# Optimization experiments

Hardware: AMD Instinct MI355X
Metric: run time of the kernel (lower is better)

The kernel has to match this reference:

```python
import jax, jax.numpy as jnp
import numpy as np

# Production-scale dims (ScanNet-like 3D instance segmentation, Mask3D-style matcher)
B = 4            # scenes per batch (equal-size segments; offset = cumulative N)
N = 65536        # points per scene
Q = 400          # instance queries
NUM_CLASSES = 20 # semantic classes
M = 64           # max GT instances per scene
COST_CLASS = 1.0
COST_MASK = 1.0
COST_DICE = 1.0


def setup_inputs() -> dict:
    key = jax.random.key(0)
    k1, k2, k3, k4 = jax.random.split(key, 4)
    outputs_mask = jax.random.normal(k1, (B, N, Q), dtype=jnp.float32)
    outputs_class = jax.random.normal(k2, (B, Q, NUM_CLASSES), dtype=jnp.float32)
    instance = jax.random.randint(k3, (B, N), 0, M, dtype=jnp.int32)
    segment = jax.random.randint(k4, (B, N), 0, NUM_CLASSES, dtype=jnp.int32)
    return {
        'outputs_mask': outputs_mask,
        'outputs_class': outputs_class,
        'instance': instance,
        'segment': segment,
    }


def _cost_matrix(out_mask_nq, out_cls, inst, seg):
    # out_mask_nq: [N, Q] mask logits; out_cls: [Q, C]; inst, seg: [N] int
    out_mask = out_mask_nq.T                      # [Q, N]
    out_seg = jax.nn.softmax(out_cls, axis=-1)    # [Q, C]

    # F.one_hot(inst + 1).T[1:] with labels in [0, M) == one_hot(inst, M).T
    tgt = jax.nn.one_hot(inst, M, dtype=jnp.float32).T  # [M, N]

    # semantic label per instance: (tgt_mask * tgt_segm).max(1)
    inst_seg = jnp.max(tgt * seg.astype(jnp.float32)[None, :], axis=1).astype(jnp.int32)  # [M]
    cost_class = 1.0 - out_seg[:, inst_seg]       # [Q, M]

    # batch_sigmoid_ce_loss: BCEwithLogits(x,1)=softplus(-x), BCEwithLogits(x,0)=softplus(x)
    inv_hw = 1.0 / N
    pos = jax.nn.softplus(-out_mask) * inv_hw     # [Q, N]
    neg = jax.nn.softplus(out_mask) * inv_hw      # [Q, N]
    cost_mask = (jnp.einsum('qn,mn->qm', pos, tgt)
                 + jnp.einsum('qn,mn->qm', neg, 1.0 - tgt))  # [Q, M]

    # batch_dice_loss
    sig = jax.nn.sigmoid(out_mask)                # [Q, N]
    numerator = 2.0 * jnp.einsum('qn,mn->qm', sig, tgt)
    denominator = sig.sum(-1)[:, None] + tgt.sum(-1)[None, :]
    cost_dice = 1.0 - (numerator + 1.0) / (denominator + 1.0)

    return COST_MASK * cost_mask + COST_CLASS * cost_class + COST_DICE * cost_dice


def reference(outputs_mask, outputs_class, instance, segment):
    # vmap over scenes (equal-size segments replace the per-batch offset loop)
    return jax.vmap(_cost_matrix)(outputs_mask, outputs_class, instance, segment)  # [B, Q, M]
```

## Files before the change

kernel.cpp:

```cpp
#include <hip/hip_runtime.h>
#include <hip/hip_bf16.h>

#define B_ 4
#define N_ 65536
#define Q_ 400
#define C_ 20
#define M_ 64
#define QT 64
#define CHUNK 1024
#define NCHUNK (N_ / CHUNK)
#define NQT ((Q_ + QT - 1) / QT)

#define SX 8192.0f
#define SS 32768.0f
#define SN 8192.0f

__global__ __launch_bounds__(256) void stats_kernel(const int* __restrict__ inst,
                                                    const int* __restrict__ seg,
                                                    int* __restrict__ cnt_g,
                                                    int* __restrict__ smax_g) {
    int b = blockIdx.x >> 4;
    int chunk = blockIdx.x & 15;
    __shared__ int scnt[M_];
    __shared__ int smax[M_];
    int tid = threadIdx.x;
    if (tid < M_) { scnt[tid] = 0; smax[tid] = 0; }
    __syncthreads();
    int base = b * N_ + chunk * 4096;
    for (int i = 0; i < 4096; i += 256) {
        int m = inst[base + tid + i];
        int s = seg[base + tid + i];
        atomicAdd(&scnt[m], 1);
        atomicMax(&smax[m], s);
    }
    __syncthreads();
    if (tid < M_) {
        atomicAdd(&cnt_g[b * M_ + tid], scnt[tid]);
        atomicMax(&smax_g[b * M_ + tid], smax[tid]);
    }
}

__global__ __launch_bounds__(512) void bin_kernel(const float* __restrict__ mask,
                                                  const int* __restrict__ inst,
                                                  int* __restrict__ xsum,
                                                  int* __restrict__ ssum,
                                                  int* __restrict__ negsum) {
    int chunk = blockIdx.x, qt = blockIdx.y, b = blockIdx.z;
    int qbase = qt * QT;
    __shared__ int xs[M_][QT + 1];
    __shared__ int ss[M_][QT + 1];
    __shared__ int linst[CHUNK];
    int tid = threadIdx.x;
    for (int i = tid; i < M_ * (QT + 1); i += 512) {
        (&xs[0][0])[i] = 0;
        (&ss[0][0])[i] = 0;
    }
    const int2* ip = (const int2*)(inst + b * N_ + chunk * CHUNK);
    ((int2*)linst)[tid] = ip[tid];
    __syncthreads();

    int lane = tid & 63, wave = tid >> 6;
    int r = lane >> 4, c = lane & 15;
    int q0 = qbase + 4 * c;
    bool qok = (q0 < Q_);
    int lq = 4 * c;

    float n0 = 0.f, n1 = 0.f, n2 = 0.f, n3 = 0.f;
    int lnbase = wave * 4 + r;
    const float* mbase = mask + ((size_t)b * N_ + (size_t)chunk * CHUNK) * Q_ + q0;

    if (qok) {
        for (int i = 0; i < CHUNK / 32; i += 2) {
            int ln0 = lnbase + i * 32;
            int ln1 = ln0 + 32;
            float4 xa = *(const float4*)(mbase + (size_t)ln0 * Q_);
            float4 xb = *(const float4*)(mbase + (size_t)ln1 * Q_);
            int m0 = linst[ln0];
            int m1 = linst[ln1];

            float ea0 = __expf(xa.x), ea1 = __expf(xa.y), ea2 = __expf(xa.z), ea3 = __expf(xa.w);
            float eb0 = __expf(xb.x), eb1 = __expf(xb.y), eb2 = __expf(xb.z), eb3 = __expf(xb.w);
            float ta0 = 1.f + ea0, ta1 = 1.f + ea1, ta2 = 1.f + ea2, ta3 = 1.f + ea3;
            float tb0 = 1.f + eb0, tb1 = 1.f + eb1, tb2 = 1.f + eb2, tb3 = 1.f + eb3;
            float sa0 = ea0 * __builtin_amdgcn_rcpf(ta0);
            float sa1 = ea1 * __builtin_amdgcn_rcpf(ta1);
            float sa2 = ea2 * __builtin_amdgcn_rcpf(ta2);
            float sa3 = ea3 * __builtin_amdgcn_rcpf(ta3);
            float sb0 = eb0 * __builtin_amdgcn_rcpf(tb0);
            float sb1 = eb1 * __builtin_amdgcn_rcpf(tb1);
            float sb2 = eb2 * __builtin_amdgcn_rcpf(tb2);
            float sb3 = eb3 * __builtin_amdgcn_rcpf(tb3);

            atomicAdd(&xs[m0][lq + 0], __float2int_rn(xa.x * SX));
            atomicAdd(&xs[m0][lq + 1], __float2int_rn(xa.y * SX));
            atomicAdd(&xs[m0][lq + 2], __float2int_rn(xa.z * SX));
            atomicAdd(&xs[m0][lq + 3], __float2int_rn(xa.w * SX));
            atomicAdd(&ss[m0][lq + 0], (int)__float2uint_rn(sa0 * SS));
            atomicAdd(&ss[m0][lq + 1], (int)__float2uint_rn(sa1 * SS));
            atomicAdd(&ss[m0][lq + 2], (int)__float2uint_rn(sa2 * SS));
            atomicAdd(&ss[m0][lq + 3], (int)__float2uint_rn(sa3 * SS));
            atomicAdd(&xs[m1][lq + 0], __float2int_rn(xb.x * SX));
            atomicAdd(&xs[m1][lq + 1], __float2int_rn(xb.y * SX));
            atomicAdd(&xs[m1][lq + 2], __float2int_rn(xb.z * SX));
            atomicAdd(&xs[m1][lq + 3], __float2int_rn(xb.w * SX));
            atomicAdd(&ss[m1][lq + 0], (int)__float2uint_rn(sb0 * SS));
            atomicAdd(&ss[m1][lq + 1], (int)__float2uint_rn(sb1 * SS));
            atomicAdd(&ss[m1][lq + 2], (int)__float2uint_rn(sb2 * SS));
            atomicAdd(&ss[m1][lq + 3], (int)__float2uint_rn(sb3 * SS));

            n0 += __logf(ta0) + __logf(tb0);
            n1 += __logf(ta1) + __logf(tb1);
            n2 += __logf(ta2) + __logf(tb2);
            n3 += __logf(ta3) + __logf(tb3);
        }
    }

    n0 += __shfl_xor(n0, 16); n0 += __shfl_xor(n0, 32);
    n1 += __shfl_xor(n1, 16); n1 += __shfl_xor(n1, 32);
    n2 += __shfl_xor(n2, 16); n2 += __shfl_xor(n2, 32);
    n3 += __shfl_xor(n3, 16); n3 += __shfl_xor(n3, 32);
    if (r == 0 && qok) {
        atomicAdd(&negsum[b * Q_ + q0 + 0], __float2int_rn(n0 * SN));
        atomicAdd(&negsum[b * Q_ + q0 + 1], __float2int_rn(n1 * SN));
        atomicAdd(&negsum[b * Q_ + q0 + 2], __float2int_rn(n2 * SN));
        atomicAdd(&negsum[b * Q_ + q0 + 3], __float2int_rn(n3 * SN));
    }
    __syncthreads();

    for (int idx = tid; idx < M_ * QT; idx += 512) {
        int m = idx & (M_ - 1);
        int lqq = idx >> 6;
        int q = qbase + lqq;
        if (q < Q_) {
            atomicAdd(&xsum[((b * Q_ + q) << 6) + m], xs[m][lqq]);
            atomicAdd(&ssum[((b * Q_ + q) << 6) + m], ss[m][lqq]);
        }
    }
}

__global__ __launch_bounds__(64) void final_kernel(const float* __restrict__ cls_in,
                                                   const int* __restrict__ xsum,
                                                   const int* __restrict__ ssum,
                                                   const int* __restrict__ negsum,
                                                   const int* __restrict__ cnt_g,
                                                   const int* __restrict__ smax_g,
                                                   float* __restrict__ out) {
    int bq = blockIdx.x;
    int b = bq / Q_;
    int m = threadIdx.x;
    float Xs = (float)xsum[(bq << 6) + m] * (1.0f / SX);
    float Ss = (float)ssum[(bq << 6) + m] * (1.0f / SS);
    float sigsum = Ss;
    for (int off = 32; off; off >>= 1) sigsum += __shfl_xor(sigsum, off);

    __shared__ float cls[C_];
    if (m < C_) cls[m] = cls_in[bq * C_ + m];
    __syncthreads();
    float mx = cls[0];
    for (int i = 1; i < C_; ++i) mx = fmaxf(mx, cls[i]);
    float se = 0.f;
    for (int i = 0; i < C_; ++i) se += __expf(cls[i] - mx);
    int label = smax_g[b * M_ + m];
    float p = __expf(cls[label] - mx) / se;

    float negf = (float)negsum[bq] * (1.0f / SN);
    float cm = (negf - Xs) * (1.f / (float)N_);
    float cd = 1.f - (2.f * Ss + 1.f) / (sigsum + (float)cnt_g[b * M_ + m] + 1.f);
    out[(bq << 6) + m] = cm + (1.f - p) + cd;
}

extern "C" void kernel_launch(void* const* d_in, const int* in_sizes, int n_in,
                              void* d_out, int out_size, void* d_ws, size_t ws_size,
                              hipStream_t stream) {
    const float* mask = (const float*)d_in[0];
    const float* cls  = (const float*)d_in[1];
    const int*   inst = (const int*)d_in[2];
    const int*   seg  = (const int*)d_in[3];
    float* out = (float*)d_out;

    int* xsum   = (int*)d_ws;
    int* ssum   = xsum + B_ * Q_ * M_;
    int* negsum = ssum + B_ * Q_ * M_;
    int* cnt_g  = negsum + B_ * Q_;
    int* smax_g = cnt_g + B_ * M_;

    size_t zbytes = (size_t)(2 * B_ * Q_ * M_ + B_ * Q_ + 2 * B_ * M_) * 4;
    hipMemsetAsync(d_ws, 0, zbytes, stream);

    stats_kernel<<<B_ * 16, 256, 0, stream>>>(inst, seg, cnt_g, smax_g);
    bin_kernel<<<dim3(NCHUNK, NQT, B_), 512, 0, stream>>>(mask, inst, xsum, ssum, negsum);
    final_kernel<<<B_ * Q_, 64, 0, stream>>>(cls, xsum, ssum, negsum, cnt_g, smax_g, out);
}
```

Before: 644.2 us.

## Counting-sort points by instance per chunk to replace LDS atomics with register reductions

```diff
diff --git a/kernel.cpp b/kernel.cpp
--- a/kernel.cpp
+++ b/kernel.cpp
@@ -7,133 +7,169 @@
 #define C_ 20
 #define M_ 64
 #define QT 64
-#define CHUNK 1024
+#define CHUNK 2048
 #define NCHUNK (N_ / CHUNK)
 #define NQT ((Q_ + QT - 1) / QT)
+#define OFFSTRIDE (M_ + 2)
 
 #define SX 8192.0f
 #define SS 32768.0f
 #define SN 8192.0f
 
-__global__ __launch_bounds__(256) void stats_kernel(const int* __restrict__ inst,
-                                                    const int* __restrict__ seg,
-                                                    int* __restrict__ cnt_g,
-                                                    int* __restrict__ smax_g) {
-    int b = blockIdx.x >> 4;
-    int chunk = blockIdx.x & 15;
-    __shared__ int scnt[M_];
+__global__ __launch_bounds__(256) void sort_kernel(const int* __restrict__ inst,
+                                                   const int* __restrict__ seg,
+                                                   unsigned short* __restrict__ perm,
+                                                   int* __restrict__ binoff,
+                                                   int* __restrict__ cnt_g,
+                                                   int* __restrict__ smax_g) {
+    int b = blockIdx.x >> 5;
+    int chunk = blockIdx.x & 31;
+    __shared__ int hist[M_];
     __shared__ int smax[M_];
+    __shared__ int cur[M_];
+    __shared__ int off[M_ + 1];
+    __shared__ unsigned short lperm[CHUNK];
     int tid = threadIdx.x;
-    if (tid < M_) { scnt[tid] = 0; smax[tid] = 0; }
-    __syncthreads();
-    int base = b * N_ + chunk * 4096;
-    for (int i = 0; i < 4096; i += 256) {
-        int m = inst[base + tid + i];
-        int s = seg[base + tid + i];
-        atomicAdd(&scnt[m], 1);
+    if (tid < M_) { hist[tid] = 0; smax[tid] = 0; }
+    __syncthreads();
+
+    int base = b * N_ + chunk * CHUNK;
+    int mloc[CHUNK / 256];
+#pragma unroll
+    for (int i = 0; i < CHUNK / 256; ++i) {
+        int idx = tid + i * 256;
+        int m = inst[base + idx];
+        int s = seg[base + idx];
+        mloc[i] = m;
+        atomicAdd(&hist[m], 1);
         atomicMax(&smax[m], s);
     }
     __syncthreads();
+
+    if (tid == 0) {
+        int acc = 0;
+        for (int m = 0; m < M_; ++m) { off[m] = acc; acc += hist[m]; }
+        off[M_] = acc;
+    }
+    __syncthreads();
+    if (tid < M_) cur[tid] = off[tid];
+    __syncthreads();
+
+#pragma unroll
+    for (int i = 0; i < CHUNK / 256; ++i) {
+        int idx = tid + i * 256;
+        int pos = atomicAdd(&cur[mloc[i]], 1);
+        lperm[pos] = (unsigned short)idx;
+    }
+    __syncthreads();
+
+    unsigned int* pg = (unsigned int*)(perm + ((size_t)b * NCHUNK + chunk) * CHUNK);
+    const unsigned int* pl = (const unsigned int*)lperm;
+    for (int i = tid; i < CHUNK / 2; i += 256) pg[i] = pl[i];
+
+    int obase = (b * NCHUNK + chunk) * OFFSTRIDE;
+    if (tid <= M_) binoff[obase + tid] = off[tid];
     if (tid < M_) {
-        atomicAdd(&cnt_g[b * M_ + tid], scnt[tid]);
+        atomicAdd(&cnt_g[b * M_ + tid], hist[tid]);
         atomicMax(&smax_g[b * M_ + tid], smax[tid]);
     }
 }
 
 __global__ __launch_bounds__(512) void bin_kernel(const float* __restrict__ mask,
-                                                  const int* __restrict__ inst,
+                                                  const unsigned short* __restrict__ perm,
+                                                  const int* __restrict__ binoff,
                                                   int* __restrict__ xsum,
                                                   int* __restrict__ ssum,
                                                   int* __restrict__ negsum) {
     int chunk = blockIdx.x, qt = blockIdx.y, b = blockIdx.z;
-    int qbase = qt * QT;
-    __shared__ int xs[M_][QT + 1];
-    __shared__ int ss[M_][QT + 1];
-    __shared__ int linst[CHUNK];
+    __shared__ unsigned short lperm[CHUNK];
+    __shared__ int loff[M_ + 1];
     int tid = threadIdx.x;
-    for (int i = tid; i < M_ * (QT + 1); i += 512) {
-        (&xs[0][0])[i] = 0;
-        (&ss[0][0])[i] = 0;
-    }
-    const int2* ip = (const int2*)(inst + b * N_ + chunk * CHUNK);
-    ((int2*)linst)[tid] = ip[tid];
+
+    const unsigned int* pg = (const unsigned int*)(perm + ((size_t)b * NCHUNK + chunk) * CHUNK);
+    unsigned int* pl = (unsigned int*)lperm;
+    for (int i = tid; i < CHUNK / 2; i += 512) pl[i] = pg[i];
+    if (tid <= M_) loff[tid] = binoff[(b * NCHUNK + chunk) * OFFSTRIDE + tid];
     __syncthreads();
 
     int lane = tid & 63, wave = tid >> 6;
     int r = lane >> 4, c = lane & 15;
-    int q0 = qbase + 4 * c;
+    int q0 = qt * QT + 4 * c;
     bool qok = (q0 < Q_);
-    int lq = 4 * c;
-
+    const float* mbase = mask + ((size_t)b * N_ + (size_t)chunk * CHUNK) * Q_ + q0;
     float n0 = 0.f, n1 = 0.f, n2 = 0.f, n3 = 0.f;
-    int lnbase = wave * 4 + r;
-    const float* mbase = mask + ((size_t)b * N_ + (size_t)chunk * CHUNK) * Q_ + q0;
 
     if (qok) {
-        for (int i = 0; i < CHUNK / 32; i += 2) {
-            int ln0 = lnbase + i * 32;
-            int ln1 = ln0 + 32;
-            float4 xa = *(const float4*)(mbase + (size_t)ln0 * Q_);
-            float4 xb = *(const float4*)(mbase + (size_t)ln1 * Q_);
-            int m0 = linst[ln0];
-            int m1 = linst[ln1];
-
-            float ea0 = __expf(xa.x), ea1 = __expf(xa.y), ea2 = __expf(xa.z), ea3 = __expf(xa.w);
-            float eb0 = __expf(xb.x), eb1 = __expf(xb.y), eb2 = __expf(xb.z), eb3 = __expf(xb.w);
-            float ta0 = 1.f + ea0, ta1 = 1.f + ea1, ta2 = 1.f + ea2, ta3 = 1.f + ea3;
-            float tb0 = 1.f + eb0, tb1 = 1.f + eb1, tb2 = 1.f + eb2, tb3 = 1.f + eb3;
-            float sa0 = ea0 * __builtin_amdgcn_rcpf(ta0);
-            float sa1 = ea1 * __builtin_amdgcn_rcpf(ta1);
-            float sa2 = ea2 * __builtin_amdgcn_rcpf(ta2);
-            float sa3 = ea3 * __builtin_amdgcn_rcpf(ta3);
-            float sb0 = eb0 * __builtin_amdgcn_rcpf(tb0);
-            float sb1 = eb1 * __builtin_amdgcn_rcpf(tb1);
-            float sb2 = eb2 * __builtin_amdgcn_rcpf(tb2);
-            float sb3 = eb3 * __builtin_amdgcn_rcpf(tb3);
-
-            atomicAdd(&xs[m0][lq + 0], __float2int_rn(xa.x * SX));
-            atomicAdd(&xs[m0][lq + 1], __float2int_rn(xa.y * SX));
-            atomicAdd(&xs[m0][lq + 2], __float2int_rn(xa.z * SX));
-            atomicAdd(&xs[m0][lq + 3], __float2int_rn(xa.w * SX));
-            atomicAdd(&ss[m0][lq + 0], (int)__float2uint_rn(sa0 * SS));
-            atomicAdd(&ss[m0][lq + 1], (int)__float2uint_rn(sa1 * SS));
-            atomicAdd(&ss[m0][lq + 2], (int)__float2uint_rn(sa2 * SS));
-            atomicAdd(&ss[m0][lq + 3], (int)__float2uint_rn(sa3 * SS));
-            atomicAdd(&xs[m1][lq + 0], __float2int_rn(xb.x * SX));
-            atomicAdd(&xs[m1][lq + 1], __float2int_rn(xb.y * SX));
-            atomicAdd(&xs[m1][lq + 2], __float2int_rn(xb.z * SX));
-            atomicAdd(&xs[m1][lq + 3], __float2int_rn(xb.w * SX));
-            atomicAdd(&ss[m1][lq + 0], (int)__float2uint_rn(sb0 * SS));
-            atomicAdd(&ss[m1][lq + 1], (int)__float2uint_rn(sb1 * SS));
-            atomicAdd(&ss[m1][lq + 2], (int)__float2uint_rn(sb2 * SS));
-            atomicAdd(&ss[m1][lq + 3], (int)__float2uint_rn(sb3 * SS));
-
-            n0 += __logf(ta0) + __logf(tb0);
-            n1 += __logf(ta1) + __logf(tb1);
-            n2 += __logf(ta2) + __logf(tb2);
-            n3 += __logf(ta3) + __logf(tb3);
+        for (int k = 0; k < M_ / 8; ++k) {
+            int m = wave + 8 * k;
+            int s = loff[m], e = loff[m + 1];
+            float x0 = 0.f, x1 = 0.f, x2 = 0.f, x3 = 0.f;
+            float g0 = 0.f, g1 = 0.f, g2 = 0.f, g3 = 0.f;
+            int pos = s + r;
+            for (; pos + 4 < e; pos += 8) {
+                int na = lperm[pos];
+                int nb = lperm[pos + 4];
+                float4 xa = *(const float4*)(mbase + (size_t)na * Q_);
+                float4 xb = *(const float4*)(mbase + (size_t)nb * Q_);
+
+                float ea0 = __expf(xa.x), ea1 = __expf(xa.y), ea2 = __expf(xa.z), ea3 = __expf(xa.w);
+                float eb0 = __expf(xb.x), eb1 = __expf(xb.y), eb2 = __expf(xb.z), eb3 = __expf(xb.w);
+                float ta0 = 1.f + ea0, ta1 = 1.f + ea1, ta2 = 1.f + ea2, ta3 = 1.f + ea3;
+                float tb0 = 1.f + eb0, tb1 = 1.f + eb1, tb2 = 1.f + eb2, tb3 = 1.f + eb3;
+
+                x0 += xa.x + xb.x; x1 += xa.y + xb.y;
+                x2 += xa.z + xb.z; x3 += xa.w + xb.w;
+                g0 += ea0 * __builtin_amdgcn_rcpf(ta0) + eb0 * __builtin_amdgcn_rcpf(tb0);
+                g1 += ea1 * __builtin_amdgcn_rcpf(ta1) + eb1 * __builtin_amdgcn_rcpf(tb1);
+                g2 += ea2 * __builtin_amdgcn_rcpf(ta2) + eb2 * __builtin_amdgcn_rcpf(tb2);
+                g3 += ea3 * __builtin_amdgcn_rcpf(ta3) + eb3 * __builtin_amdgcn_rcpf(tb3);
+                n0 += __logf(ta0) + __logf(tb0);
+                n1 += __logf(ta1) + __logf(tb1);
+                n2 += __logf(ta2) + __logf(tb2);
+                n3 += __logf(ta3) + __logf(tb3);
+            }
+            if (pos < e) {
+                int na = lperm[pos];
+                float4 xa = *(const float4*)(mbase + (size_t)na * Q_);
+                float ea0 = __expf(xa.x), ea1 = __expf(xa.y), ea2 = __expf(xa.z), ea3 = __expf(xa.w);
+                float ta0 = 1.f + ea0, ta1 = 1.f + ea1, ta2 = 1.f + ea2, ta3 = 1.f + ea3;
+                x0 += xa.x; x1 += xa.y; x2 += xa.z; x3 += xa.w;
+                g0 += ea0 * __builtin_amdgcn_rcpf(ta0);
+                g1 += ea1 * __builtin_amdgcn_rcpf(ta1);
+                g2 += ea2 * __builtin_amdgcn_rcpf(ta2);
+                g3 += ea3 * __builtin_amdgcn_rcpf(ta3);
+                n0 += __logf(ta0); n1 += __logf(ta1);
+                n2 += __logf(ta2); n3 += __logf(ta3);
+            }
+            x0 += __shfl_xor(x0, 16); x0 += __shfl_xor(x0, 32);
+            x1 += __shfl_xor(x1, 16); x1 += __shfl_xor(x1, 32);
+            x2 += __shfl_xor(x2, 16); x2 += __shfl_xor(x2, 32);
+            x3 += __shfl_xor(x3, 16); x3 += __shfl_xor(x3, 32);
+            g0 += __shfl_xor(g0, 16); g0 += __shfl_xor(g0, 32);
+            g1 += __shfl_xor(g1, 16); g1 += __shfl_xor(g1, 32);
+            g2 += __shfl_xor(g2, 16); g2 += __shfl_xor(g2, 32);
+            g3 += __shfl_xor(g3, 16); g3 += __shfl_xor(g3, 32);
+            if (r == 0) {
+                int bq = ((b * Q_ + q0) << 6) + m;
+                atomicAdd(&xsum[bq + (0 << 6)], __float2int_rn(x0 * SX));
+                atomicAdd(&xsum[bq + (1 << 6)], __float2int_rn(x1 * SX));
+                atomicAdd(&xsum[bq + (2 << 6)], __float2int_rn(x2 * SX));
+                atomicAdd(&xsum[bq + (3 << 6)], __float2int_rn(x3 * SX));
+                atomicAdd(&ssum[bq + (0 << 6)], (int)__float2uint_rn(g0 * SS));
+                atomicAdd(&ssum[bq + (1 << 6)], (int)__float2uint_rn(g1 * SS));
+                atomicAdd(&ssum[bq + (2 << 6)], (int)__float2uint_rn(g2 * SS));
+                atomicAdd(&ssum[bq + (3 << 6)], (int)__float2uint_rn(g3 * SS));
+            }
         }
-    }
-
-    n0 += __shfl_xor(n0, 16); n0 += __shfl_xor(n0, 32);
-    n1 += __shfl_xor(n1, 16); n1 += __shfl_xor(n1, 32);
-    n2 += __shfl_xor(n2, 16); n2 += __shfl_xor(n2, 32);
-    n3 += __shfl_xor(n3, 16); n3 += __shfl_xor(n3, 32);
-    if (r == 0 && qok) {
-        atomicAdd(&negsum[b * Q_ + q0 + 0], __float2int_rn(n0 * SN));
-        atomicAdd(&negsum[b * Q_ + q0 + 1], __float2int_rn(n1 * SN));
-        atomicAdd(&negsum[b * Q_ + q0 + 2], __float2int_rn(n2 * SN));
-        atomicAdd(&negsum[b * Q_ + q0 + 3], __float2int_rn(n3 * SN));
-    }
-    __syncthreads();
-
-    for (int idx = tid; idx < M_ * QT; idx += 512) {
-        int m = idx & (M_ - 1);
-        int lqq = idx >> 6;
-        int q = qbase + lqq;
-        if (q < Q_) {
-            atomicAdd(&xsum[((b * Q_ + q) << 6) + m], xs[m][lqq]);
-            atomicAdd(&ssum[((b * Q_ + q) << 6) + m], ss[m][lqq]);
+        n0 += __shfl_xor(n0, 16); n0 += __shfl_xor(n0, 32);
+        n1 += __shfl_xor(n1, 16); n1 += __shfl_xor(n1, 32);
+        n2 += __shfl_xor(n2, 16); n2 += __shfl_xor(n2, 32);
+        n3 += __shfl_xor(n3, 16); n3 += __shfl_xor(n3, 32);
+        if (r == 0) {
+            atomicAdd(&negsum[b * Q_ + q0 + 0], __float2int_rn(n0 * SN));
+            atomicAdd(&negsum[b * Q_ + q0 + 1], __float2int_rn(n1 * SN));
+            atomicAdd(&negsum[b * Q_ + q0 + 2], __float2int_rn(n2 * SN));
+            atomicAdd(&negsum[b * Q_ + q0 + 3], __float2int_rn(n3 * SN));
         }
     }
 }
@@ -183,11 +219,13 @@
     int* negsum = ssum + B_ * Q_ * M_;
     int* cnt_g  = negsum + B_ * Q_;
     int* smax_g = cnt_g + B_ * M_;
+    int* binoff = smax_g + B_ * M_;
+    unsigned short* perm = (unsigned short*)(binoff + B_ * NCHUNK * OFFSTRIDE);
 
     size_t zbytes = (size_t)(2 * B_ * Q_ * M_ + B_ * Q_ + 2 * B_ * M_) * 4;
     hipMemsetAsync(d_ws, 0, zbytes, stream);
 
-    stats_kernel<<<B_ * 16, 256, 0, stream>>>(inst, seg, cnt_g, smax_g);
-    bin_kernel<<<dim3(NCHUNK, NQT, B_), 512, 0, stream>>>(mask, inst, xsum, ssum, negsum);
+    sort_kernel<<<B_ * NCHUNK, 256, 0, stream>>>(inst, seg, perm, binoff, cnt_g, smax_g);
+    bin_kernel<<<dim3(NCHUNK, NQT, B_), 512, 0, stream>>>(mask, perm, binoff, xsum, ssum, negsum);
     final_kernel<<<B_ * Q_, 64, 0, stream>>>(cls, xsum, ssum, negsum, cnt_g, smax_g, out);
 }
```

After: 752.1 us. 16.8% more time.
